# Kernel optimization log

Measured on AMD Instinct MI355X. Metric: run time of the kernel, lower is better.

Reference implementation:

```python
import jax, jax.numpy as jnp
import numpy as np

N_NODES = 50000
N_EDGES = 800000
NUM_RADIAL = 16
HIDDEN = 128


def setup_inputs() -> dict:
    key = jax.random.key(0)
    ks = jax.random.split(key, 9)
    return {
        "x": jax.random.randint(ks[0], (N_NODES,), 0, 100),
        "rbf": jax.random.normal(ks[1], (N_EDGES, NUM_RADIAL), dtype=jnp.float32),
        "i": jax.random.randint(ks[2], (N_EDGES,), 0, N_NODES),
        "j": jax.random.randint(ks[3], (N_EDGES,), 0, N_NODES),
        "emb": jax.random.normal(ks[4], (100, HIDDEN), dtype=jnp.float32),
        "W_rbf": jax.random.normal(ks[5], (HIDDEN, NUM_RADIAL), dtype=jnp.float32) * 0.1,
        "b_rbf": jax.random.normal(ks[6], (HIDDEN,), dtype=jnp.float32) * 0.1,
        "W_lin": jax.random.normal(ks[7], (HIDDEN, 3 * HIDDEN), dtype=jnp.float32) * 0.05,
        "b_lin": jax.random.normal(ks[8], (HIDDEN,), dtype=jnp.float32) * 0.1,
    }


def reference(x, rbf, i, j, emb, W_rbf, b_rbf, W_lin, b_lin):
    # Embed atom types: [N_nodes, H]
    h = emb[x]
    # rbf projection + activation: [E, H]
    r = jax.nn.silu(rbf @ W_rbf.T + b_rbf)
    # Gather endpoints, concat with rbf features: [E, 3H]
    cat = jnp.concatenate([h[i], h[j], r], axis=-1)
    # Final linear + activation: [E, H]
    return jax.nn.silu(cat @ W_lin.T + b_lin)
```

## Files before the change

kernel.cpp:

```cpp
#include <hip/hip_runtime.h>
#include <hip/hip_bf16.h>

#define HID  128
#define NRAD 16
#define NT   100

#define PL_BYTES   (NT * 260 * 4)
#define RB_OFF     PL_BYTES
#define AL_OFF     (RB_OFF + 128 * 256)
#define BL_OFF     (AL_OFF + 512)
#define LDS_BYTES  (BL_OFF + 512)

typedef __attribute__((ext_vector_type(4))) float f32x4;
typedef __attribute__((ext_vector_type(8))) __bf16 bf16x8;
typedef __attribute__((ext_vector_type(4))) __bf16 bf16x4;

union F8 { bf16x8 b; int4 i4; };
union B4 { bf16x4 b4; int2 i2; };

__device__ inline unsigned short f2bfbits(float f){
  unsigned int u = __float_as_uint(f);
  u += 0x7FFFu + ((u >> 16) & 1u);
  return (unsigned short)(u >> 16);
}

__device__ inline float silu_f(float v){
  return v * __builtin_amdgcn_rcpf(1.0f + __expf(-v));
}

__global__ void setup_kernel(const float* __restrict__ emb,
                             const float* __restrict__ W_lin,
                             const float* __restrict__ b_lin,
                             const float* __restrict__ W_rbf,
                             int ntypes,
                             float* __restrict__ P,
                             unsigned short* __restrict__ W3,
                             unsigned short* __restrict__ WrbfB){
  int blk = blockIdx.x;
  int n = threadIdx.x;
  if (blk < ntypes){
    __shared__ float er[HID];
    if (n < HID) er[n] = emb[blk * HID + n];
    __syncthreads();
    int half = n >> 7, nn = n & 127;
    const float4* w4 = (const float4*)(W_lin + (size_t)nn * (3 * HID) + half * HID);
    float s = half ? 0.0f : b_lin[nn];
    #pragma unroll 8
    for (int k4 = 0; k4 < HID / 4; ++k4){
      float4 w = w4[k4];
      s += er[k4*4+0]*w.x + er[k4*4+1]*w.y + er[k4*4+2]*w.z + er[k4*4+3]*w.w;
    }
    P[blk * 256 + n] = s;
  } else if (blk < ntypes + 64){
    int idx = (blk - ntypes) * 256 + n;
    int r = idx >> 7, k = idx & 127;
    W3[idx] = f2bfbits(W_lin[(size_t)r * (3 * HID) + 2 * HID + k]);
  } else {
    int idx = (blk - ntypes - 64) * 256 + n;
    WrbfB[idx] = f2bfbits(W_rbf[idx]);
  }
}

__global__ __launch_bounds__(512) void edge_kernel(
    const float* __restrict__ rbf,
    const int*   __restrict__ ei,
    const int*   __restrict__ ej,
    const int*   __restrict__ x,
    const unsigned short* __restrict__ WrbfB,
    const float* __restrict__ brbf,
    const float* __restrict__ Pg,
    const unsigned short* __restrict__ W3,
    float* __restrict__ out,
    int E, int ntile)
{
  extern __shared__ char smem[];
  float* Pl = (float*)smem;
  char*  rb = smem + RB_OFF;
  int*   aL = (int*)(smem + AL_OFF);
  int*   bL = (int*)(smem + BL_OFF);

  const int tid  = threadIdx.x;
  const int lane = tid & 63;
  const int wv   = tid >> 6;
  const int erow = lane & 15;
  const int kgrp = lane >> 4;

  for (int i = tid; i < NT * 64; i += 512){
    int row = i >> 6, c4 = i & 63;
    *(f32x4*)(Pl + row * 260 + c4 * 4) = *(const f32x4*)(Pg + row * 256 + c4 * 4);
  }

  F8 wr[8];
  #pragma unroll
  for (int t = 0; t < 8; ++t){
    wr[t].i4 = make_int4(0, 0, 0, 0);
    if (kgrp < 2) wr[t].i4 = *(const int4*)(WrbfB + (t * 16 + erow) * NRAD + kgrp * 8);
  }
  F8 w3[4];
  #pragma unroll
  for (int s = 0; s < 4; ++s)
    w3[s].i4 = *(const int4*)(W3 + (wv * 16 + erow) * HID + s * 32 + kgrp * 8);
  float4 bias[8];
  #pragma unroll
  for (int t = 0; t < 8; ++t) bias[t] = *(const float4*)(brbf + t * 16 + kgrp * 4);

  __syncthreads();

  int tile = blockIdx.x;
  int2 e2 = make_int2(0, 0), j2 = make_int2(0, 0);
  if (tid < 64 && tile < ntile){
    long i0 = (long)tile * 128 + tid * 2;
    if (i0 > E - 2) i0 = E - 2;
    e2 = *(const int2*)(ei + i0);
    j2 = *(const int2*)(ej + i0);
  }
  f32x4 f0 = {0,0,0,0}, f1 = {0,0,0,0};
  if (tile < ntile && kgrp < 2){
    long ge = (long)tile * 128 + wv * 16 + erow;
    if (ge < E){
      const f32x4* s4 = (const f32x4*)(rbf + ge * NRAD + kgrp * 8);
      f0 = __builtin_nontemporal_load(s4);
      f1 = __builtin_nontemporal_load(s4 + 1);
    }
  }

  while (tile < ntile){
    const long base = (long)tile * 128;
    const int  next = tile + gridDim.x;

    if (tid < 64){
      int2 av, bv;
      av.x = x[e2.x]; av.y = x[e2.y];
      bv.x = x[j2.x]; bv.y = x[j2.y];
      *(int2*)(aL + tid * 2) = av;
      *(int2*)(bL + tid * 2) = bv;
      if (next < ntile){
        long i0 = (long)next * 128 + tid * 2;
        if (i0 > E - 2) i0 = E - 2;
        e2 = *(const int2*)(ei + i0);
        j2 = *(const int2*)(ej + i0);
      }
    }

    f32x4 nf0 = {0,0,0,0}, nf1 = {0,0,0,0};
    if (next < ntile && kgrp < 2){
      long gn = (long)next * 128 + wv * 16 + erow;
      if (gn < E){
        const f32x4* s4 = (const f32x4*)(rbf + gn * NRAD + kgrp * 8);
        nf0 = __builtin_nontemporal_load(s4);
        nf1 = __builtin_nontemporal_load(s4 + 1);
      }
    }

    const int e_l = wv * 16 + erow;
    F8 fb; fb.i4 = make_int4(0, 0, 0, 0);
    if (kgrp < 2){
      fb.b[0]=(__bf16)f0.x; fb.b[1]=(__bf16)f0.y; fb.b[2]=(__bf16)f0.z; fb.b[3]=(__bf16)f0.w;
      fb.b[4]=(__bf16)f1.x; fb.b[5]=(__bf16)f1.y; fb.b[6]=(__bf16)f1.z; fb.b[7]=(__bf16)f1.w;
    }
    #pragma unroll
    for (int t = 0; t < 8; ++t){
      f32x4 acc = {0.f, 0.f, 0.f, 0.f};
      acc = __builtin_amdgcn_mfma_f32_16x16x32_bf16(wr[t].b, fb.b, acc, 0, 0, 0);
      B4 pk;
      pk.b4[0] = (__bf16)silu_f(acc[0] + bias[t].x);
      pk.b4[1] = (__bf16)silu_f(acc[1] + bias[t].y);
      pk.b4[2] = (__bf16)silu_f(acc[2] + bias[t].z);
      pk.b4[3] = (__bf16)silu_f(acc[3] + bias[t].w);
      int byte = (e_l << 8) + t * 32 + kgrp * 8;
      byte ^= (e_l & 7) << 4;
      *(int2*)(rb + byte) = pk.i2;
    }

    asm volatile("s_waitcnt lgkmcnt(0)" ::: "memory");
    __builtin_amdgcn_s_barrier();

    const int nb = wv * 16 + kgrp * 4;
    #pragma unroll
    for (int eg = 0; eg < 8; ++eg){
      const int ed = eg * 16 + erow;
      f32x4 acc = {0.f, 0.f, 0.f, 0.f};
      #pragma unroll
      for (int s = 0; s < 4; ++s){
        int byte = (ed << 8) + s * 64 + kgrp * 16;
        byte ^= (ed & 7) << 4;
        F8 bB; bB.i4 = *(const int4*)(rb + byte);
        acc = __builtin_amdgcn_mfma_f32_16x16x32_bf16(w3[s].b, bB.b, acc, 0, 0, 0);
      }
      int a = aL[ed], b = bL[ed];
      f32x4 p1 = *(const f32x4*)(Pl + a * 260 + nb);
      f32x4 p2 = *(const f32x4*)(Pl + b * 260 + 128 + nb);
      f32x4 o;
      o.x = silu_f(acc[0] + p1.x + p2.x);
      o.y = silu_f(acc[1] + p1.y + p2.y);
      o.z = silu_f(acc[2] + p1.z + p2.z);
      o.w = silu_f(acc[3] + p1.w + p2.w);
      long ge = base + ed;
      if (ge < E)
        *(f32x4*)(out + ge * HID + nb) = o;
    }

    asm volatile("s_waitcnt lgkmcnt(0)" ::: "memory");
    __builtin_amdgcn_s_barrier();

    f0 = nf0; f1 = nf1;
    tile = next;
  }
}

extern "C" void kernel_launch(void* const* d_in, const int* in_sizes, int n_in,
                              void* d_out, int out_size, void* d_ws, size_t ws_size,
                              hipStream_t stream){
  const int*   x    = (const int*)  d_in[0];
  const float* rbf  = (const float*)d_in[1];
  const int*   ei   = (const int*)  d_in[2];
  const int*   ej   = (const int*)  d_in[3];
  const float* emb  = (const float*)d_in[4];
  const float* Wrbf = (const float*)d_in[5];
  const float* brbf = (const float*)d_in[6];
  const float* Wlin = (const float*)d_in[7];
  const float* blin = (const float*)d_in[8];
  float* out = (float*)d_out;

  const int E      = in_sizes[2];
  const int ntypes = in_sizes[4] / HID;

  float*          P     = (float*)d_ws;
  unsigned short* W3    = (unsigned short*)((char*)d_ws + (size_t)ntypes * 256 * sizeof(float));
  unsigned short* WrbfB = (unsigned short*)((char*)W3 + (size_t)HID * HID * sizeof(unsigned short));

  setup_kernel<<<ntypes + 64 + 8, 256, 0, stream>>>(emb, Wlin, blin, Wrbf, ntypes, P, W3, WrbfB);

  (void)hipFuncSetAttribute(reinterpret_cast<const void*>(&edge_kernel),
                            hipFuncAttributeMaxDynamicSharedMemorySize, LDS_BYTES);

  const int ntile = (E + 127) / 128;
  const int nblk  = ntile < 256 ? ntile : 256;
  edge_kernel<<<nblk, 512, LDS_BYTES, stream>>>(rbf, ei, ej, x, WrbfB, brbf, P, W3, out, E, ntile);
}
```

Before: 133.5 us.

## Double-buffer LDS tiles, store node projections as bf16, prefetch type lookups a tile ahead

Stores the per-type projection table in bf16 (halving its LDS footprint and the upfront copy) so the rbf-activation tile and index buffers can be double-buffered. This drops the trailing barrier per tile. The dependent x[i]/x[j] type lookups are now issued one tile ahead to hide gather latency. It loses precision on the node projection terms and adds LDS usage.

```diff
diff --git a/kernel.cpp b/kernel.cpp
--- a/kernel.cpp
+++ b/kernel.cpp
@@ -5,11 +5,11 @@
 #define NRAD 16
 #define NT   100
 
-#define PL_BYTES   (NT * 260 * 4)
+#define PL_BYTES   (NT * 260 * 2)
 #define RB_OFF     PL_BYTES
-#define AL_OFF     (RB_OFF + 128 * 256)
-#define BL_OFF     (AL_OFF + 512)
-#define LDS_BYTES  (BL_OFF + 512)
+#define AL_OFF     (RB_OFF + 2 * 128 * 256)
+#define BL_OFF     (AL_OFF + 2 * 512)
+#define LDS_BYTES  (BL_OFF + 2 * 512)
 
 typedef __attribute__((ext_vector_type(4))) float f32x4;
 typedef __attribute__((ext_vector_type(8))) __bf16 bf16x8;
@@ -27,13 +27,16 @@
 __device__ inline float silu_f(float v){
   return v * __builtin_amdgcn_rcpf(1.0f + __expf(-v));
 }
+
+__device__ inline float bflo(int q){ return __uint_as_float((unsigned)q << 16); }
+__device__ inline float bfhi(int q){ return __uint_as_float((unsigned)q & 0xFFFF0000u); }
 
 __global__ void setup_kernel(const float* __restrict__ emb,
                              const float* __restrict__ W_lin,
                              const float* __restrict__ b_lin,
                              const float* __restrict__ W_rbf,
                              int ntypes,
-                             float* __restrict__ P,
+                             unsigned short* __restrict__ Pbf,
                              unsigned short* __restrict__ W3,
                              unsigned short* __restrict__ WrbfB){
   int blk = blockIdx.x;
@@ -50,7 +53,8 @@
       float4 w = w4[k4];
       s += er[k4*4+0]*w.x + er[k4*4+1]*w.y + er[k4*4+2]*w.z + er[k4*4+3]*w.w;
     }
-    P[blk * 256 + n] = s;
+    Pbf[blk * 260 + n] = f2bfbits(s);
+    if (n < 4) Pbf[blk * 260 + 256 + n] = 0;
   } else if (blk < ntypes + 64){
     int idx = (blk - ntypes) * 256 + n;
     int r = idx >> 7, k = idx & 127;
@@ -68,27 +72,25 @@
     const int*   __restrict__ x,
     const unsigned short* __restrict__ WrbfB,
     const float* __restrict__ brbf,
-    const float* __restrict__ Pg,
+    const unsigned short* __restrict__ Pbf,
     const unsigned short* __restrict__ W3,
     float* __restrict__ out,
     int E, int ntile)
 {
   extern __shared__ char smem[];
-  float* Pl = (float*)smem;
-  char*  rb = smem + RB_OFF;
-  int*   aL = (int*)(smem + AL_OFF);
-  int*   bL = (int*)(smem + BL_OFF);
+  char*  rb  = smem + RB_OFF;
+  int*   aL  = (int*)(smem + AL_OFF);
+  int*   bL  = (int*)(smem + BL_OFF);
 
   const int tid  = threadIdx.x;
   const int lane = tid & 63;
   const int wv   = tid >> 6;
   const int erow = lane & 15;
   const int kgrp = lane >> 4;
-
-  for (int i = tid; i < NT * 64; i += 512){
-    int row = i >> 6, c4 = i & 63;
-    *(f32x4*)(Pl + row * 260 + c4 * 4) = *(const f32x4*)(Pg + row * 256 + c4 * 4);
-  }
+  const int G    = gridDim.x;
+
+  for (int i = tid; i < PL_BYTES / 16; i += 512)
+    ((int4*)smem)[i] = ((const int4*)Pbf)[i];
 
   F8 wr[8];
   #pragma unroll
@@ -104,18 +106,25 @@
   #pragma unroll
   for (int t = 0; t < 8; ++t) bias[t] = *(const float4*)(brbf + t * 16 + kgrp * 4);
 
-  __syncthreads();
-
   int tile = blockIdx.x;
-  int2 e2 = make_int2(0, 0), j2 = make_int2(0, 0);
-  if (tid < 64 && tile < ntile){
+  int2 xa = make_int2(0,0), xb = make_int2(0,0);
+  int2 e2 = make_int2(0,0), j2 = make_int2(0,0);
+  if (tid < 64){
     long i0 = (long)tile * 128 + tid * 2;
     if (i0 > E - 2) i0 = E - 2;
-    e2 = *(const int2*)(ei + i0);
-    j2 = *(const int2*)(ej + i0);
+    int2 t0 = *(const int2*)(ei + i0);
+    int2 t1 = *(const int2*)(ej + i0);
+    xa.x = x[t0.x]; xa.y = x[t0.y];
+    xb.x = x[t1.x]; xb.y = x[t1.y];
+    if (tile + G < ntile){
+      long i1 = (long)(tile + G) * 128 + tid * 2;
+      if (i1 > E - 2) i1 = E - 2;
+      e2 = *(const int2*)(ei + i1);
+      j2 = *(const int2*)(ej + i1);
+    }
   }
   f32x4 f0 = {0,0,0,0}, f1 = {0,0,0,0};
-  if (tile < ntile && kgrp < 2){
+  if (kgrp < 2){
     long ge = (long)tile * 128 + wv * 16 + erow;
     if (ge < E){
       const f32x4* s4 = (const f32x4*)(rbf + ge * NRAD + kgrp * 8);
@@ -124,21 +133,28 @@
     }
   }
 
+  __syncthreads();
+
+  int buf = 0;
   while (tile < ntile){
     const long base = (long)tile * 128;
-    const int  next = tile + gridDim.x;
+    const int  next = tile + G;
+    char* rbc = rb + buf * 32768;
+    int*  aLc = aL + buf * 128;
+    int*  bLc = bL + buf * 128;
 
     if (tid < 64){
-      int2 av, bv;
-      av.x = x[e2.x]; av.y = x[e2.y];
-      bv.x = x[j2.x]; bv.y = x[j2.y];
-      *(int2*)(aL + tid * 2) = av;
-      *(int2*)(bL + tid * 2) = bv;
+      *(int2*)(aLc + tid * 2) = xa;
+      *(int2*)(bLc + tid * 2) = xb;
       if (next < ntile){
-        long i0 = (long)next * 128 + tid * 2;
-        if (i0 > E - 2) i0 = E - 2;
-        e2 = *(const int2*)(ei + i0);
-        j2 = *(const int2*)(ej + i0);
+        xa.x = x[e2.x]; xa.y = x[e2.y];
+        xb.x = x[j2.x]; xb.y = x[j2.y];
+        if (next + G < ntile){
+          long i1 = (long)(next + G) * 128 + tid * 2;
+          if (i1 > E - 2) i1 = E - 2;
+          e2 = *(const int2*)(ei + i1);
+          j2 = *(const int2*)(ej + i1);
+        }
       }
     }
 
@@ -169,13 +185,14 @@
       pk.b4[3] = (__bf16)silu_f(acc[3] + bias[t].w);
       int byte = (e_l << 8) + t * 32 + kgrp * 8;
       byte ^= (e_l & 7) << 4;
-      *(int2*)(rb + byte) = pk.i2;
+      *(int2*)(rbc + byte) = pk.i2;
     }
 
     asm volatile("s_waitcnt lgkmcnt(0)" ::: "memory");
     __builtin_amdgcn_s_barrier();
 
     const int nb = wv * 16 + kgrp * 4;
+    const unsigned short* PlU = (const unsigned short*)smem;
     #pragma unroll
     for (int eg = 0; eg < 8; ++eg){
       const int ed = eg * 16 + erow;
@@ -184,26 +201,24 @@
       for (int s = 0; s < 4; ++s){
         int byte = (ed << 8) + s * 64 + kgrp * 16;
         byte ^= (ed & 7) << 4;
-        F8 bB; bB.i4 = *(const int4*)(rb + byte);
+        F8 bB; bB.i4 = *(const int4*)(rbc + byte);
         acc = __builtin_amdgcn_mfma_f32_16x16x32_bf16(w3[s].b, bB.b, acc, 0, 0, 0);
       }
-      int a = aL[ed], b = bL[ed];
-      f32x4 p1 = *(const f32x4*)(Pl + a * 260 + nb);
-      f32x4 p2 = *(const f32x4*)(Pl + b * 260 + 128 + nb);
+      int a = aLc[ed], b = bLc[ed];
+      int2 q1 = *(const int2*)(PlU + a * 260 + nb);
+      int2 q2 = *(const int2*)(PlU + b * 260 + 128 + nb);
       f32x4 o;
-      o.x = silu_f(acc[0] + p1.x + p2.x);
-      o.y = silu_f(acc[1] + p1.y + p2.y);
-      o.z = silu_f(acc[2] + p1.z + p2.z);
-      o.w = silu_f(acc[3] + p1.w + p2.w);
+      o.x = silu_f(acc[0] + bflo(q1.x) + bflo(q2.x));
+      o.y = silu_f(acc[1] + bfhi(q1.x) + bfhi(q2.x));
+      o.z = silu_f(acc[2] + bflo(q1.y) + bflo(q2.y));
+      o.w = silu_f(acc[3] + bfhi(q1.y) + bfhi(q2.y));
       long ge = base + ed;
       if (ge < E)
         *(f32x4*)(out + ge * HID + nb) = o;
     }
 
-    asm volatile("s_waitcnt lgkmcnt(0)" ::: "memory");
-    __builtin_amdgcn_s_barrier();
-
     f0 = nf0; f1 = nf1;
+    buf ^= 1;
     tile = next;
   }
 }
@@ -225,16 +240,16 @@
   const int E      = in_sizes[2];
   const int ntypes = in_sizes[4] / HID;
 
-  float*          P     = (float*)d_ws;
-  unsigned short* W3    = (unsigned short*)((char*)d_ws + (size_t)ntypes * 256 * sizeof(float));
+  unsigned short* Pbf   = (unsigned short*)d_ws;
+  unsigned short* W3    = (unsigned short*)((char*)d_ws + PL_BYTES);
   unsigned short* WrbfB = (unsigned short*)((char*)W3 + (size_t)HID * HID * sizeof(unsigned short));
 
-  setup_kernel<<<ntypes + 64 + 8, 256, 0, stream>>>(emb, Wlin, blin, Wrbf, ntypes, P, W3, WrbfB);
+  setup_kernel<<<ntypes + 64 + 8, 256, 0, stream>>>(emb, Wlin, blin, Wrbf, ntypes, Pbf, W3, WrbfB);
 
   (void)hipFuncSetAttribute(reinterpret_cast<const void*>(&edge_kernel),
                             hipFuncAttributeMaxDynamicSharedMemorySize, LDS_BYTES);
 
   const int ntile = (E + 127) / 128;
   const int nblk  = ntile < 256 ? ntile : 256;
-  edge_kernel<<<nblk, 512, LDS_BYTES, stream>>>(rbf, ei, ej, x, WrbfB, brbf, P, W3, out, E, ntile);
-}
+  edge_kernel<<<nblk, 512, LDS_BYTES, stream>>>(rbf, ei, ej, x, WrbfB, brbf, Pbf, W3, out, E, ntile);
+}
```

Result: slower. 143.5 us (+7.5%).

## Precompute per-edge atom types in setup and remap waves to 2 output tiles

Applied to the files above, without the earlier changes.

The setup kernel now resolves x[i] and x[j] for every edge into a packed int2 array in workspace. Each edge-kernel wave then loads these types directly in registers, which removes the per-tile LDS staging and one of the two barriers' dependencies on the dependent gather chain. The second GEMM is remapped so each wave covers 64 edges by 32 output features with two accumulators, reusing each LDS B fragment twice. The cost is a larger setup kernel with an extra pass over the edge indices, more weight registers per wave, and a fallback path when the workspace is too small.

```diff
diff --git a/kernel.cpp b/kernel.cpp
--- a/kernel.cpp
+++ b/kernel.cpp
@@ -7,9 +7,12 @@
 
 #define PL_BYTES   (NT * 260 * 4)
 #define RB_OFF     PL_BYTES
-#define AL_OFF     (RB_OFF + 128 * 256)
-#define BL_OFF     (AL_OFF + 512)
-#define LDS_BYTES  (BL_OFF + 512)
+#define LDS_BYTES  (RB_OFF + 128 * 256)
+
+#define WS_P_BYTES   (NT * 256 * 4)
+#define WS_W3_OFF    WS_P_BYTES
+#define WS_WRBF_OFF  (WS_W3_OFF + HID * HID * 2)
+#define WS_XIJ_OFF   (WS_WRBF_OFF + HID * NRAD * 2 + 1920)
 
 typedef __attribute__((ext_vector_type(4))) float f32x4;
 typedef __attribute__((ext_vector_type(8))) __bf16 bf16x8;
@@ -32,10 +35,14 @@
                              const float* __restrict__ W_lin,
                              const float* __restrict__ b_lin,
                              const float* __restrict__ W_rbf,
-                             int ntypes,
+                             const int*   __restrict__ ei,
+                             const int*   __restrict__ ej,
+                             const int*   __restrict__ x,
+                             int ntypes, int E,
                              float* __restrict__ P,
                              unsigned short* __restrict__ W3,
-                             unsigned short* __restrict__ WrbfB){
+                             unsigned short* __restrict__ WrbfB,
+                             int2* __restrict__ xij){
   int blk = blockIdx.x;
   int n = threadIdx.x;
   if (blk < ntypes){
@@ -55,9 +62,21 @@
     int idx = (blk - ntypes) * 256 + n;
     int r = idx >> 7, k = idx & 127;
     W3[idx] = f2bfbits(W_lin[(size_t)r * (3 * HID) + 2 * HID + k]);
-  } else {
+  } else if (blk < ntypes + 72){
     int idx = (blk - ntypes - 64) * 256 + n;
     WrbfB[idx] = f2bfbits(W_rbf[idx]);
+  } else {
+    int idx = (blk - ntypes - 72) * 512 + n * 2;
+    if (idx + 1 < E){
+      int2 e2 = *(const int2*)(ei + idx);
+      int2 j2 = *(const int2*)(ej + idx);
+      int4 v;
+      v.x = x[e2.x]; v.y = x[j2.x];
+      v.z = x[e2.y]; v.w = x[j2.y];
+      *(int4*)(xij + idx) = v;
+    } else if (idx < E){
+      xij[idx] = make_int2(x[ei[idx]], x[ej[idx]]);
+    }
   }
 }
 
@@ -70,20 +89,22 @@
     const float* __restrict__ brbf,
     const float* __restrict__ Pg,
     const unsigned short* __restrict__ W3,
+    const int2*  __restrict__ xij,
     float* __restrict__ out,
-    int E, int ntile)
+    int E, int ntile, int use_xij)
 {
   extern __shared__ char smem[];
   float* Pl = (float*)smem;
   char*  rb = smem + RB_OFF;
-  int*   aL = (int*)(smem + AL_OFF);
-  int*   bL = (int*)(smem + BL_OFF);
 
   const int tid  = threadIdx.x;
   const int lane = tid & 63;
   const int wv   = tid >> 6;
   const int erow = lane & 15;
   const int kgrp = lane >> 4;
+  const int gg   = wv >> 2;
+  const int ww   = wv & 3;
+  const int G    = gridDim.x;
 
   for (int i = tid; i < NT * 64; i += 512){
     int row = i >> 6, c4 = i & 63;
@@ -96,24 +117,17 @@
     wr[t].i4 = make_int4(0, 0, 0, 0);
     if (kgrp < 2) wr[t].i4 = *(const int4*)(WrbfB + (t * 16 + erow) * NRAD + kgrp * 8);
   }
-  F8 w3[4];
+  F8 w3[8];
   #pragma unroll
-  for (int s = 0; s < 4; ++s)
-    w3[s].i4 = *(const int4*)(W3 + (wv * 16 + erow) * HID + s * 32 + kgrp * 8);
+  for (int u = 0; u < 2; ++u)
+    #pragma unroll
+    for (int s = 0; s < 4; ++s)
+      w3[u*4+s].i4 = *(const int4*)(W3 + ((ww*2+u)*16 + erow) * HID + s * 32 + kgrp * 8);
   float4 bias[8];
   #pragma unroll
   for (int t = 0; t < 8; ++t) bias[t] = *(const float4*)(brbf + t * 16 + kgrp * 4);
 
-  __syncthreads();
-
   int tile = blockIdx.x;
-  int2 e2 = make_int2(0, 0), j2 = make_int2(0, 0);
-  if (tid < 64 && tile < ntile){
-    long i0 = (long)tile * 128 + tid * 2;
-    if (i0 > E - 2) i0 = E - 2;
-    e2 = *(const int2*)(ei + i0);
-    j2 = *(const int2*)(ej + i0);
-  }
   f32x4 f0 = {0,0,0,0}, f1 = {0,0,0,0};
   if (tile < ntile && kgrp < 2){
     long ge = (long)tile * 128 + wv * 16 + erow;
@@ -124,21 +138,22 @@
     }
   }
 
+  __syncthreads();
+
   while (tile < ntile){
     const long base = (long)tile * 128;
-    const int  next = tile + gridDim.x;
-
-    if (tid < 64){
-      int2 av, bv;
-      av.x = x[e2.x]; av.y = x[e2.y];
-      bv.x = x[j2.x]; bv.y = x[j2.y];
-      *(int2*)(aL + tid * 2) = av;
-      *(int2*)(bL + tid * 2) = bv;
-      if (next < ntile){
-        long i0 = (long)next * 128 + tid * 2;
-        if (i0 > E - 2) i0 = E - 2;
-        e2 = *(const int2*)(ei + i0);
-        j2 = *(const int2*)(ej + i0);
+    const int  next = tile + G;
+
+    int2 xv[4];
+    #pragma unroll
+    for (int eg = 0; eg < 4; ++eg){
+      long ge = base + gg * 64 + eg * 16 + erow;
+      if (ge > E - 1) ge = E - 1;
+      if (use_xij){
+        xv[eg] = xij[ge];
+      } else {
+        xv[eg].x = x[ei[ge]];
+        xv[eg].y = x[ej[ge]];
       }
     }
 
@@ -175,29 +190,34 @@
     asm volatile("s_waitcnt lgkmcnt(0)" ::: "memory");
     __builtin_amdgcn_s_barrier();
 
-    const int nb = wv * 16 + kgrp * 4;
-    #pragma unroll
-    for (int eg = 0; eg < 8; ++eg){
-      const int ed = eg * 16 + erow;
-      f32x4 acc = {0.f, 0.f, 0.f, 0.f};
+    #pragma unroll
+    for (int eg = 0; eg < 4; ++eg){
+      const int ed = gg * 64 + eg * 16 + erow;
+      f32x4 a0 = {0.f,0.f,0.f,0.f}, a1 = {0.f,0.f,0.f,0.f};
       #pragma unroll
       for (int s = 0; s < 4; ++s){
         int byte = (ed << 8) + s * 64 + kgrp * 16;
         byte ^= (ed & 7) << 4;
         F8 bB; bB.i4 = *(const int4*)(rb + byte);
-        acc = __builtin_amdgcn_mfma_f32_16x16x32_bf16(w3[s].b, bB.b, acc, 0, 0, 0);
-      }
-      int a = aL[ed], b = bL[ed];
-      f32x4 p1 = *(const f32x4*)(Pl + a * 260 + nb);
-      f32x4 p2 = *(const f32x4*)(Pl + b * 260 + 128 + nb);
-      f32x4 o;
-      o.x = silu_f(acc[0] + p1.x + p2.x);
-      o.y = silu_f(acc[1] + p1.y + p2.y);
-      o.z = silu_f(acc[2] + p1.z + p2.z);
-      o.w = silu_f(acc[3] + p1.w + p2.w);
-      long ge = base + ed;
-      if (ge < E)
-        *(f32x4*)(out + ge * HID + nb) = o;
+        a0 = __builtin_amdgcn_mfma_f32_16x16x32_bf16(w3[s].b,   bB.b, a0, 0, 0, 0);
+        a1 = __builtin_amdgcn_mfma_f32_16x16x32_bf16(w3[4+s].b, bB.b, a1, 0, 0, 0);
+      }
+      const int aT = xv[eg].x, bT = xv[eg].y;
+      const long ge = base + ed;
+      #pragma unroll
+      for (int u = 0; u < 2; ++u){
+        f32x4 acc = u ? a1 : a0;
+        int nb = (ww * 2 + u) * 16 + kgrp * 4;
+        f32x4 p1 = *(const f32x4*)(Pl + aT * 260 + nb);
+        f32x4 p2 = *(const f32x4*)(Pl + bT * 260 + 128 + nb);
+        f32x4 o;
+        o.x = silu_f(acc[0] + p1.x + p2.x);
+        o.y = silu_f(acc[1] + p1.y + p2.y);
+        o.z = silu_f(acc[2] + p1.z + p2.z);
+        o.w = silu_f(acc[3] + p1.w + p2.w);
+        if (ge < E)
+          *(f32x4*)(out + ge * HID + nb) = o;
+      }
     }
 
     asm volatile("s_waitcnt lgkmcnt(0)" ::: "memory");
@@ -226,15 +246,23 @@
   const int ntypes = in_sizes[4] / HID;
 
   float*          P     = (float*)d_ws;
-  unsigned short* W3    = (unsigned short*)((char*)d_ws + (size_t)ntypes * 256 * sizeof(float));
-  unsigned short* WrbfB = (unsigned short*)((char*)W3 + (size_t)HID * HID * sizeof(unsigned short));
-
-  setup_kernel<<<ntypes + 64 + 8, 256, 0, stream>>>(emb, Wlin, blin, Wrbf, ntypes, P, W3, WrbfB);
+  unsigned short* W3    = (unsigned short*)((char*)d_ws + WS_P_BYTES);
+  unsigned short* WrbfB = (unsigned short*)((char*)d_ws + WS_P_BYTES + HID * HID * 2);
+  size_t xij_off = (size_t)WS_P_BYTES + HID * HID * 2 + HID * NRAD * 2;
+  xij_off = (xij_off + 15) & ~(size_t)15;
+  int2* xij = (int2*)((char*)d_ws + xij_off);
+
+  const int use_xij = (ws_size >= xij_off + (size_t)E * 8) ? 1 : 0;
+  const int nxe = use_xij ? (E + 511) / 512 : 0;
+
+  setup_kernel<<<ntypes + 72 + nxe, 256, 0, stream>>>(
+      emb, Wlin, blin, Wrbf, ei, ej, x, ntypes, E, P, W3, WrbfB, xij);
 
   (void)hipFuncSetAttribute(reinterpret_cast<const void*>(&edge_kernel),
                             hipFuncAttributeMaxDynamicSharedMemorySize, LDS_BYTES);
 
   const int ntile = (E + 127) / 128;
   const int nblk  = ntile < 256 ? ntile : 256;
-  edge_kernel<<<nblk, 512, LDS_BYTES, stream>>>(rbf, ei, ej, x, WrbfB, brbf, P, W3, out, E, ntile);
-}
+  edge_kernel<<<nblk, 512, LDS_BYTES, stream>>>(
+      rbf, ei, ej, x, WrbfB, brbf, P, W3, use_xij ? xij : nullptr, out, E, ntile, use_xij);
+}
```

Result: slower. 141.1 us (+5.7%).

## Make each wave own its edges end to end, removing block barriers

Applied to the files above, without the earlier changes.

Each wave now computes the second GEMM for its own 16 edges across all 128 outputs, keeping the whole W3 matrix in registers (32 bf16x8 fragments). The rbf intermediate therefore stays wave-private in LDS, and both per-tile block barriers are gone. The rbf bias is folded into the first MFMA through a constant-1 input column. Each lane now gathers its own node types, prefetched one tile ahead, and P is written pre-padded so it can be copied straight into LDS. The cost is much higher register pressure, with launch_bounds(512,2) now requesting two blocks per CU, and the output stores change their access pattern.

```diff
diff --git a/kernel.cpp b/kernel.cpp
--- a/kernel.cpp
+++ b/kernel.cpp
@@ -7,9 +7,10 @@
 
 #define PL_BYTES   (NT * 260 * 4)
 #define RB_OFF     PL_BYTES
-#define AL_OFF     (RB_OFF + 128 * 256)
-#define BL_OFF     (AL_OFF + 512)
-#define LDS_BYTES  (BL_OFF + 512)
+#define LDS_BYTES  (RB_OFF + 128 * 256)
+
+#define WS_W3_OFF   PL_BYTES
+#define WS_WR_OFF   (WS_W3_OFF + HID * HID * 2)
 
 typedef __attribute__((ext_vector_type(4))) float f32x4;
 typedef __attribute__((ext_vector_type(8))) __bf16 bf16x8;
@@ -32,10 +33,11 @@
                              const float* __restrict__ W_lin,
                              const float* __restrict__ b_lin,
                              const float* __restrict__ W_rbf,
+                             const float* __restrict__ b_rbf,
                              int ntypes,
                              float* __restrict__ P,
                              unsigned short* __restrict__ W3,
-                             unsigned short* __restrict__ WrbfB){
+                             unsigned short* __restrict__ Wr32){
   int blk = blockIdx.x;
   int n = threadIdx.x;
   if (blk < ntypes){
@@ -50,24 +52,26 @@
       float4 w = w4[k4];
       s += er[k4*4+0]*w.x + er[k4*4+1]*w.y + er[k4*4+2]*w.z + er[k4*4+3]*w.w;
     }
-    P[blk * 256 + n] = s;
+    P[blk * 260 + n] = s;
+    if (n < 4) P[blk * 260 + 256 + n] = 0.f;
   } else if (blk < ntypes + 64){
     int idx = (blk - ntypes) * 256 + n;
     int r = idx >> 7, k = idx & 127;
     W3[idx] = f2bfbits(W_lin[(size_t)r * (3 * HID) + 2 * HID + k]);
   } else {
     int idx = (blk - ntypes - 64) * 256 + n;
-    WrbfB[idx] = f2bfbits(W_rbf[idx]);
+    int r = idx >> 5, k = idx & 31;
+    float v = (k < 16) ? W_rbf[r * NRAD + k] : (k == 16 ? b_rbf[r] : 0.f);
+    Wr32[idx] = f2bfbits(v);
   }
 }
 
-__global__ __launch_bounds__(512) void edge_kernel(
+__global__ __launch_bounds__(512, 2) void edge_kernel(
     const float* __restrict__ rbf,
     const int*   __restrict__ ei,
     const int*   __restrict__ ej,
     const int*   __restrict__ x,
-    const unsigned short* __restrict__ WrbfB,
-    const float* __restrict__ brbf,
+    const unsigned short* __restrict__ Wr32,
     const float* __restrict__ Pg,
     const unsigned short* __restrict__ W3,
     float* __restrict__ out,
@@ -76,134 +80,115 @@
   extern __shared__ char smem[];
   float* Pl = (float*)smem;
   char*  rb = smem + RB_OFF;
-  int*   aL = (int*)(smem + AL_OFF);
-  int*   bL = (int*)(smem + BL_OFF);
 
   const int tid  = threadIdx.x;
   const int lane = tid & 63;
   const int wv   = tid >> 6;
   const int erow = lane & 15;
   const int kgrp = lane >> 4;
-
-  for (int i = tid; i < NT * 64; i += 512){
-    int row = i >> 6, c4 = i & 63;
-    *(f32x4*)(Pl + row * 260 + c4 * 4) = *(const f32x4*)(Pg + row * 256 + c4 * 4);
-  }
+  const int e_l  = wv * 16 + erow;
+  const int G    = gridDim.x;
+
+  for (int i = tid; i < PL_BYTES / 16; i += 512)
+    ((int4*)smem)[i] = ((const int4*)Pg)[i];
 
   F8 wr[8];
   #pragma unroll
-  for (int t = 0; t < 8; ++t){
-    wr[t].i4 = make_int4(0, 0, 0, 0);
-    if (kgrp < 2) wr[t].i4 = *(const int4*)(WrbfB + (t * 16 + erow) * NRAD + kgrp * 8);
+  for (int t = 0; t < 8; ++t)
+    wr[t].i4 = *(const int4*)(Wr32 + (t * 16 + erow) * 32 + kgrp * 8);
+
+  F8 w3r[32];
+  #pragma unroll
+  for (int t = 0; t < 8; ++t)
+    #pragma unroll
+    for (int s = 0; s < 4; ++s)
+      w3r[t * 4 + s].i4 = *(const int4*)(W3 + (t * 16 + erow) * HID + s * 32 + kgrp * 8);
+
+  int tile = blockIdx.x;
+  long g0 = (long)tile * 128 + e_l; if (g0 > (long)E - 1) g0 = E - 1;
+  int xa = x[ei[g0]];
+  int xb = x[ej[g0]];
+  f32x4 f0 = {0,0,0,0}, f1 = {0,0,0,0};
+  if (kgrp < 2){
+    const f32x4* s4 = (const f32x4*)(rbf + g0 * NRAD + kgrp * 8);
+    f0 = __builtin_nontemporal_load(s4);
+    f1 = __builtin_nontemporal_load(s4 + 1);
   }
-  F8 w3[4];
-  #pragma unroll
-  for (int s = 0; s < 4; ++s)
-    w3[s].i4 = *(const int4*)(W3 + (wv * 16 + erow) * HID + s * 32 + kgrp * 8);
-  float4 bias[8];
-  #pragma unroll
-  for (int t = 0; t < 8; ++t) bias[t] = *(const float4*)(brbf + t * 16 + kgrp * 4);
 
   __syncthreads();
-
-  int tile = blockIdx.x;
-  int2 e2 = make_int2(0, 0), j2 = make_int2(0, 0);
-  if (tid < 64 && tile < ntile){
-    long i0 = (long)tile * 128 + tid * 2;
-    if (i0 > E - 2) i0 = E - 2;
-    e2 = *(const int2*)(ei + i0);
-    j2 = *(const int2*)(ej + i0);
-  }
-  f32x4 f0 = {0,0,0,0}, f1 = {0,0,0,0};
-  if (tile < ntile && kgrp < 2){
-    long ge = (long)tile * 128 + wv * 16 + erow;
-    if (ge < E){
-      const f32x4* s4 = (const f32x4*)(rbf + ge * NRAD + kgrp * 8);
-      f0 = __builtin_nontemporal_load(s4);
-      f1 = __builtin_nontemporal_load(s4 + 1);
-    }
-  }
 
   while (tile < ntile){
     const long base = (long)tile * 128;
-    const int  next = tile + gridDim.x;
-
-    if (tid < 64){
-      int2 av, bv;
-      av.x = x[e2.x]; av.y = x[e2.y];
-      bv.x = x[j2.x]; bv.y = x[j2.y];
-      *(int2*)(aL + tid * 2) = av;
-      *(int2*)(bL + tid * 2) = bv;
-      if (next < ntile){
-        long i0 = (long)next * 128 + tid * 2;
-        if (i0 > E - 2) i0 = E - 2;
-        e2 = *(const int2*)(ei + i0);
-        j2 = *(const int2*)(ej + i0);
-      }
-    }
-
+    const long ge   = base + e_l;
+    const int  next = tile + G;
+
+    long gn = (long)next * 128 + e_l; if (gn > (long)E - 1) gn = E - 1;
+    int nai = ei[gn];
+    int naj = ej[gn];
     f32x4 nf0 = {0,0,0,0}, nf1 = {0,0,0,0};
-    if (next < ntile && kgrp < 2){
-      long gn = (long)next * 128 + wv * 16 + erow;
-      if (gn < E){
-        const f32x4* s4 = (const f32x4*)(rbf + gn * NRAD + kgrp * 8);
-        nf0 = __builtin_nontemporal_load(s4);
-        nf1 = __builtin_nontemporal_load(s4 + 1);
-      }
-    }
-
-    const int e_l = wv * 16 + erow;
+    if (kgrp < 2){
+      const f32x4* s4 = (const f32x4*)(rbf + gn * NRAD + kgrp * 8);
+      nf0 = __builtin_nontemporal_load(s4);
+      nf1 = __builtin_nontemporal_load(s4 + 1);
+    }
+
     F8 fb; fb.i4 = make_int4(0, 0, 0, 0);
     if (kgrp < 2){
       fb.b[0]=(__bf16)f0.x; fb.b[1]=(__bf16)f0.y; fb.b[2]=(__bf16)f0.z; fb.b[3]=(__bf16)f0.w;
       fb.b[4]=(__bf16)f1.x; fb.b[5]=(__bf16)f1.y; fb.b[6]=(__bf16)f1.z; fb.b[7]=(__bf16)f1.w;
+    } else if (kgrp == 2){
+      fb.b[0] = (__bf16)1.0f;
     }
     #pragma unroll
     for (int t = 0; t < 8; ++t){
       f32x4 acc = {0.f, 0.f, 0.f, 0.f};
       acc = __builtin_amdgcn_mfma_f32_16x16x32_bf16(wr[t].b, fb.b, acc, 0, 0, 0);
       B4 pk;
-      pk.b4[0] = (__bf16)silu_f(acc[0] + bias[t].x);
-      pk.b4[1] = (__bf16)silu_f(acc[1] + bias[t].y);
-      pk.b4[2] = (__bf16)silu_f(acc[2] + bias[t].z);
-      pk.b4[3] = (__bf16)silu_f(acc[3] + bias[t].w);
+      pk.b4[0] = (__bf16)silu_f(acc[0]);
+      pk.b4[1] = (__bf16)silu_f(acc[1]);
+      pk.b4[2] = (__bf16)silu_f(acc[2]);
+      pk.b4[3] = (__bf16)silu_f(acc[3]);
       int byte = (e_l << 8) + t * 32 + kgrp * 8;
       byte ^= (e_l & 7) << 4;
       *(int2*)(rb + byte) = pk.i2;
     }
 
+    int nxa = x[nai];
+    int nxb = x[naj];
+
     asm volatile("s_waitcnt lgkmcnt(0)" ::: "memory");
-    __builtin_amdgcn_s_barrier();
-
-    const int nb = wv * 16 + kgrp * 4;
-    #pragma unroll
-    for (int eg = 0; eg < 8; ++eg){
-      const int ed = eg * 16 + erow;
-      f32x4 acc = {0.f, 0.f, 0.f, 0.f};
+
+    f32x4 acc2[8];
+    #pragma unroll
+    for (int t = 0; t < 8; ++t) acc2[t] = (f32x4){0.f, 0.f, 0.f, 0.f};
+
+    #pragma unroll
+    for (int s = 0; s < 4; ++s){
+      int byte = (e_l << 8) + s * 64 + kgrp * 16;
+      byte ^= (e_l & 7) << 4;
+      F8 bB; bB.i4 = *(const int4*)(rb + byte);
       #pragma unroll
-      for (int s = 0; s < 4; ++s){
-        int byte = (ed << 8) + s * 64 + kgrp * 16;
-        byte ^= (ed & 7) << 4;
-        F8 bB; bB.i4 = *(const int4*)(rb + byte);
-        acc = __builtin_amdgcn_mfma_f32_16x16x32_bf16(w3[s].b, bB.b, acc, 0, 0, 0);
-      }
-      int a = aL[ed], b = bL[ed];
-      f32x4 p1 = *(const f32x4*)(Pl + a * 260 + nb);
-      f32x4 p2 = *(const f32x4*)(Pl + b * 260 + 128 + nb);
+      for (int t = 0; t < 8; ++t)
+        acc2[t] = __builtin_amdgcn_mfma_f32_16x16x32_bf16(w3r[t*4+s].b, bB.b, acc2[t], 0, 0, 0);
+    }
+
+    const float* pa = Pl + xa * 260;
+    const float* pb = Pl + xb * 260 + 128;
+    #pragma unroll
+    for (int t = 0; t < 8; ++t){
+      int nb = t * 16 + kgrp * 4;
+      f32x4 p1 = *(const f32x4*)(pa + nb);
+      f32x4 p2 = *(const f32x4*)(pb + nb);
       f32x4 o;
-      o.x = silu_f(acc[0] + p1.x + p2.x);
-      o.y = silu_f(acc[1] + p1.y + p2.y);
-      o.z = silu_f(acc[2] + p1.z + p2.z);
-      o.w = silu_f(acc[3] + p1.w + p2.w);
-      long ge = base + ed;
+      o.x = silu_f(acc2[t][0] + p1.x + p2.x);
+      o.y = silu_f(acc2[t][1] + p1.y + p2.y);
+      o.z = silu_f(acc2[t][2] + p1.z + p2.z);
+      o.w = silu_f(acc2[t][3] + p1.w + p2.w);
       if (ge < E)
         *(f32x4*)(out + ge * HID + nb) = o;
     }
 
-    asm volatile("s_waitcnt lgkmcnt(0)" ::: "memory");
-    __builtin_amdgcn_s_barrier();
-
-    f0 = nf0; f1 = nf1;
+    f0 = nf0; f1 = nf1; xa = nxa; xb = nxb;
     tile = next;
   }
 }
@@ -225,16 +210,18 @@
   const int E      = in_sizes[2];
   const int ntypes = in_sizes[4] / HID;
 
-  float*          P     = (float*)d_ws;
-  unsigned short* W3    = (unsigned short*)((char*)d_ws + (size_t)ntypes * 256 * sizeof(float));
-  unsigned short* WrbfB = (unsigned short*)((char*)W3 + (size_t)HID * HID * sizeof(unsigned short));
-
-  setup_kernel<<<ntypes + 64 + 8, 256, 0, stream>>>(emb, Wlin, blin, Wrbf, ntypes, P, W3, WrbfB);
+  float*          P    = (float*)d_ws;
+  unsigned short* W3   = (unsigned short*)((char*)d_ws + WS_W3_OFF);
+  unsigned short* Wr32 = (unsigned short*)((char*)d_ws + WS_WR_OFF);
+
+  setup_kernel<<<ntypes + 64 + 16, 256, 0, stream>>>(
+      emb, Wlin, blin, Wrbf, brbf, ntypes, P, W3, Wr32);
 
   (void)hipFuncSetAttribute(reinterpret_cast<const void*>(&edge_kernel),
                             hipFuncAttributeMaxDynamicSharedMemorySize, LDS_BYTES);
 
   const int ntile = (E + 127) / 128;
   const int nblk  = ntile < 256 ? ntile : 256;
-  edge_kernel<<<nblk, 512, LDS_BYTES, stream>>>(rbf, ei, ej, x, WrbfB, brbf, P, W3, out, E, ntile);
-}
+  edge_kernel<<<nblk, 512, LDS_BYTES, stream>>>(
+      rbf, ei, ej, x, Wr32, P, W3, out, E, ntile);
+}
```

Result: slower. 173.7 us (+30.1%).
